# Kernel tuning notes

Hardware: AMD Instinct MI355X
Metric: run time of the kernel (lower is better)

## Reference

```python
import jax, jax.numpy as jnp
import numpy as np

HIDDEN = 2560
HEADS = 32
HEAD_DIM = HIDDEN // HEADS  # 80


def setup_inputs() -> dict:
    key = jax.random.key(0)
    ks = jax.random.split(key, 7)
    B, S, L = 2, 2048, 512
    scale = 1.0 / np.sqrt(HIDDEN)
    return {
        "hidden_states": jax.random.normal(ks[0], (B, S, HIDDEN), jnp.float32),
        "live_state": jax.random.normal(ks[1], (B, L, HIDDEN), jnp.float32),
        # nn.Linear weights stored [out, in]; y = x @ W.T
        "Wq": jax.random.normal(ks[2], (HIDDEN, HIDDEN), jnp.float32) * scale,
        "Wk": jax.random.normal(ks[3], (HIDDEN, HIDDEN), jnp.float32) * scale,
        "Wv": jax.random.normal(ks[4], (HIDDEN, HIDDEN), jnp.float32) * scale,
        "Wo": jax.random.normal(ks[5], (HIDDEN, HIDDEN), jnp.float32) * scale,
        "gate_param": jax.random.normal(ks[6], (), jnp.float32) * 0.1,
    }


def reference(hidden_states, live_state, Wq, Wk, Wv, Wo, gate_param):
    B, S, D = hidden_states.shape
    L = live_state.shape[1]
    H, Dh = HEADS, HEAD_DIM

    q = (hidden_states @ Wq.T).reshape(B, S, H, Dh).transpose(0, 2, 1, 3)  # [B,H,S,Dh]
    k = (live_state @ Wk.T).reshape(B, L, H, Dh).transpose(0, 2, 1, 3)    # [B,H,L,Dh]
    v = (live_state @ Wv.T).reshape(B, L, H, Dh).transpose(0, 2, 1, 3)    # [B,H,L,Dh]

    scale = 1.0 / np.sqrt(Dh)
    scores = jnp.einsum("bhsd,bhld->bhsl", q, k) * scale
    attn_weights = jax.nn.softmax(scores, axis=-1)                        # [B,H,S,L]
    attn_out = jnp.einsum("bhsl,bhld->bhsd", attn_weights, v)
    attn_out = attn_out.transpose(0, 2, 1, 3).reshape(B, S, D)
    attn_out = attn_out @ Wo.T

    gate = jnp.tanh(gate_param)
    output = gate * attn_out
    return output, attn_weights
```

## Files before the change

### kernel.cpp

```cpp
#include <hip/hip_runtime.h>
#include <hip/hip_fp16.h>
#include <cstdint>
#include <cstddef>

#define HID 2560
#define NH  32
#define DHD 80
#define DHP 96
#define NB  2
#define NS  2048
#define NL  512

typedef _Float16 half8_t __attribute__((ext_vector_type(8)));
typedef float f32x4_t __attribute__((ext_vector_type(4)));

__device__ __forceinline__ void gload_lds16(const __half* g, __half* l) {
  __builtin_amdgcn_global_load_lds(
      (const __attribute__((address_space(1))) unsigned int*)g,
      (__attribute__((address_space(3))) unsigned int*)l, 16, 0, 0);
}

__global__ __launch_bounds__(256) void cast_all(const float* __restrict__ X,
                                                const float* __restrict__ LS,
                                                const float* __restrict__ Wq,
                                                const float* __restrict__ Wk,
                                                const float* __restrict__ Wv,
                                                const float* __restrict__ Wo,
                                                __half* __restrict__ Xh,
                                                __half* __restrict__ Lh,
                                                __half* __restrict__ Wqh,
                                                __half* __restrict__ Wkh,
                                                __half* __restrict__ Wvh,
                                                __half* __restrict__ Woh,
                                                __half* __restrict__ Qa,
                                                __half* __restrict__ Ka) {
  const int nX = NB * NS * HID / 4, nL = NB * NL * HID / 4, nW = HID * HID / 4;
  const int ncast = nX + nL + 4 * nW;
  const int qrows = NB * NH * NS, krows = NB * NH * NL;
  const int total = ncast + qrows + krows;
  for (int i = blockIdx.x * 256 + threadIdx.x; i < total; i += gridDim.x * 256) {
    if (i < ncast) {
      const float* src; __half* dst; int off;
      if (i < nX) { src = X; dst = Xh; off = i; }
      else if (i < nX + nL) { src = LS; dst = Lh; off = i - nX; }
      else {
        int j = i - nX - nL;
        int w = j / nW; off = j - w * nW;
        src = (w == 0) ? Wq : (w == 1) ? Wk : (w == 2) ? Wv : Wo;
        dst = (w == 0) ? Wqh : (w == 1) ? Wkh : (w == 2) ? Wvh : Woh;
      }
      float4 v = ((const float4*)src)[off];
      union { __half h[4]; uint2 u; } r;
      r.h[0] = __float2half(v.x);
      r.h[1] = __float2half(v.y);
      r.h[2] = __float2half(v.z);
      r.h[3] = __float2half(v.w);
      ((uint2*)dst)[off] = r.u;
    } else {
      const int j = i - ncast;
      const uint4 z = {0, 0, 0, 0};
      uint4* p = (j < qrows)
          ? (uint4*)(Qa + (size_t)j * DHP + DHD)
          : (uint4*)(Ka + (size_t)(j - qrows) * DHP + DHD);
      p[0] = z; p[1] = z;
    }
  }
}

__device__ __forceinline__ void gemm256_core(const __half* A, const __half* Bt,
                                             int bm, int bn, __half* smem,
                                             f32x4_t (&acc)[8][4]) {
  const int K = HID;
  const int tid  = threadIdx.x;
  const int lane = tid & 63;
  const int wave = tid >> 6;
  const int wr = wave >> 2, wc = wave & 3;
  const int fr = lane & 15, kb = lane >> 4;

  const int sr = tid >> 3;
  const int sj = (tid & 7) ^ (sr & 7);
  const __half* gA = A  + (size_t)(bm * 256 + sr) * K + sj * 8;
  const __half* gB = Bt + (size_t)(bn * 256 + sr) * K + sj * 8;

  auto stage = [&](int h, int kt, int bank) {
    const __half* gbase = (h < 2) ? gA : gB;
    const int rbase = (h & 1) * 128;
#pragma unroll
    for (int i = 0; i < 2; ++i) {
      const __half* g = gbase + (size_t)(rbase + i * 64) * K + (size_t)kt * 64;
      __half* l = smem + bank * 32768 + (h < 2 ? 0 : 16384) + (rbase + i * 64) * 64 + tid * 8;
      gload_lds16(g, l);
    }
  };
  auto rdA = [&](int m, int kk, int bank) -> half8_t {
    const int row = wr * 128 + m * 16 + fr;
    const int off = row * 128 + ((kk * 64 + kb * 16) ^ ((fr & 7) << 4));
    return *(const half8_t*)((const char*)(smem + bank * 32768) + off);
  };
  auto rdB = [&](int n, int kk, int bank) -> half8_t {
    const int row = wc * 64 + n * 16 + fr;
    const int off = row * 128 + ((kk * 64 + kb * 16) ^ ((fr & 7) << 4));
    return *(const half8_t*)((const char*)(smem + bank * 32768 + 16384) + off);
  };

  half8_t af[4][2], bf[4][2];

#pragma unroll
  for (int h = 0; h < 4; ++h) stage(h, 0, 0);

  const int nk = K >> 6;
  for (int kt = 0; kt < nk; ++kt) {
    const int bk = kt & 1, nb2 = bk ^ 1;
    const bool pf = (kt + 1 < nk);

    if (pf) { stage(0, kt + 1, nb2); stage(1, kt + 1, nb2); }
    if (pf) asm volatile("s_waitcnt vmcnt(4)" ::: "memory");
    else    asm volatile("s_waitcnt vmcnt(0)" ::: "memory");
    asm volatile("s_barrier" ::: "memory");
#pragma unroll
    for (int m = 0; m < 4; ++m)
#pragma unroll
      for (int kk = 0; kk < 2; ++kk) af[m][kk] = rdA(m, kk, bk);
#pragma unroll
    for (int n = 0; n < 2; ++n)
#pragma unroll
      for (int kk = 0; kk < 2; ++kk) bf[n][kk] = rdB(n, kk, bk);
    __builtin_amdgcn_s_setprio(1);
#pragma unroll
    for (int m = 0; m < 4; ++m)
#pragma unroll
      for (int n = 0; n < 2; ++n)
#pragma unroll
        for (int kk = 0; kk < 2; ++kk)
          acc[m][n] = __builtin_amdgcn_mfma_f32_16x16x32_f16(af[m][kk], bf[n][kk], acc[m][n], 0, 0, 0);
    __builtin_amdgcn_s_setprio(0);
    asm volatile("s_barrier" ::: "memory");

#pragma unroll
    for (int n = 2; n < 4; ++n)
#pragma unroll
      for (int kk = 0; kk < 2; ++kk) bf[n][kk] = rdB(n, kk, bk);
    if (pf) stage(2, kt + 1, nb2);
    asm volatile("s_barrier" ::: "memory");
    __builtin_amdgcn_s_setprio(1);
#pragma unroll
    for (int m = 0; m < 4; ++m)
#pragma unroll
      for (int n = 2; n < 4; ++n)
#pragma unroll
        for (int kk = 0; kk < 2; ++kk)
          acc[m][n] = __builtin_amdgcn_mfma_f32_16x16x32_f16(af[m][kk], bf[n][kk], acc[m][n], 0, 0, 0);
    __builtin_amdgcn_s_setprio(0);
    asm volatile("s_barrier" ::: "memory");

#pragma unroll
    for (int m = 0; m < 4; ++m)
#pragma unroll
      for (int kk = 0; kk < 2; ++kk) af[m][kk] = rdA(m + 4, kk, bk);
    if (pf) stage(3, kt + 1, nb2);
    asm volatile("s_barrier" ::: "memory");
    __builtin_amdgcn_s_setprio(1);
#pragma unroll
    for (int m = 0; m < 4; ++m)
#pragma unroll
      for (int n = 2; n < 4; ++n)
#pragma unroll
        for (int kk = 0; kk < 2; ++kk)
          acc[m + 4][n] = __builtin_amdgcn_mfma_f32_16x16x32_f16(af[m][kk], bf[n][kk], acc[m + 4][n], 0, 0, 0);
    __builtin_amdgcn_s_setprio(0);
    asm volatile("s_barrier" ::: "memory");

    asm volatile("s_barrier" ::: "memory");
    __builtin_amdgcn_s_setprio(1);
#pragma unroll
    for (int m = 0; m < 4; ++m)
#pragma unroll
      for (int n = 0; n < 2; ++n)
#pragma unroll
        for (int kk = 0; kk < 2; ++kk)
          acc[m + 4][n] = __builtin_amdgcn_mfma_f32_16x16x32_f16(af[m][kk], bf[n][kk], acc[m + 4][n], 0, 0, 0);
    __builtin_amdgcn_s_setprio(0);
    asm volatile("s_barrier" ::: "memory");
  }
}

__global__ __launch_bounds__(512) void fused_qkv(const __half* __restrict__ X,
                                                 const __half* __restrict__ L,
                                                 const __half* __restrict__ Wq,
                                                 const __half* __restrict__ Wk,
                                                 const __half* __restrict__ Wv,
                                                 __half* __restrict__ Qa,
                                                 __half* __restrict__ Ka,
                                                 __half* __restrict__ Va) {
  __shared__ __half smem[2 * 32768];
  int wg = blockIdx.x;
  wg = (wg & 7) * 30 + (wg >> 3);

  int mode, bm, bn;
  const __half *A, *B;
  if (wg < 160)      { mode = 0; A = X; B = Wq; bm = wg / 10;        bn = wg - bm * 10; }
  else if (wg < 200) { mode = 1; A = L; B = Wk; bm = (wg - 160) / 10; bn = (wg - 160) - bm * 10; }
  else               { mode = 2; A = L; B = Wv; bm = (wg - 200) / 10; bn = (wg - 200) - bm * 10; }

  f32x4_t acc[8][4] = {};
  gemm256_core(A, B, bm, bn, smem, acc);

  const int lane = threadIdx.x & 63, wave = threadIdx.x >> 6;
  const int wr = wave >> 2, wc = wave & 3;
  const int fr = lane & 15, kb = lane >> 4;

#pragma unroll
  for (int m = 0; m < 8; ++m)
#pragma unroll
    for (int n = 0; n < 4; ++n)
#pragma unroll
      for (int r = 0; r < 4; ++r) {
        const int row = bm * 256 + wr * 128 + m * 16 + kb * 4 + r;
        const int col = bn * 256 + wc * 64 + n * 16 + fr;
        const float v = acc[m][n][r];
        const int h = col / DHD, d = col - h * DHD;
        if (mode == 0) {
          const int b = row >> 11, s = row & 2047;
          Qa[(((size_t)(b * NH + h)) * NS + s) * DHP + d] =
              __float2half(v * 0.11180339887498949f);
        } else if (mode == 1) {
          const int b = row >> 9, l = row & 511;
          Ka[(((size_t)(b * NH + h)) * NL + l) * DHP + d] = __float2half(v);
        } else {
          const int b = row >> 9, l = row & 511;
          Va[(((size_t)(b * NH + h)) * DHP + d) * NL + l] = __float2half(v);
        }
      }
}

__global__ __launch_bounds__(512) void gemm256_o(const __half* __restrict__ A,
                                                 const __half* __restrict__ Bt,
                                                 float* __restrict__ out,
                                                 const float* __restrict__ gate_p) {
  __shared__ __half smem[2 * 32768];
  int wg = blockIdx.x;
  wg = (wg & 7) * 20 + (wg >> 3);
  const int bm = wg / 10, bn = wg - bm * 10;

  f32x4_t acc[8][4] = {};
  gemm256_core(A, Bt, bm, bn, smem, acc);

  const float gate = tanhf(gate_p[0]);
  const int lane = threadIdx.x & 63, wave = threadIdx.x >> 6;
  const int wr = wave >> 2, wc = wave & 3;
  const int fr = lane & 15, kb = lane >> 4;

#pragma unroll
  for (int m = 0; m < 8; ++m)
#pragma unroll
    for (int n = 0; n < 4; ++n)
#pragma unroll
      for (int r = 0; r < 4; ++r) {
        const int row = bm * 256 + wr * 128 + m * 16 + kb * 4 + r;
        const int col = bn * 256 + wc * 64 + n * 16 + fr;
        __builtin_nontemporal_store(gate * acc[m][n][r],
                                    &out[(size_t)row * HID + col]);
      }
}

__global__ __launch_bounds__(256, 2) void attn_kernel(const __half* __restrict__ Q,
                                                      const __half* __restrict__ Kt,
                                                      const __half* __restrict__ Vt,
                                                      float* __restrict__ P,
                                                      __half* __restrict__ AO) {
  __shared__ __half Pl[4 * 16 * 520];
  __shared__ __half KV[6144];
  const int tid = threadIdx.x;
  const int lane = tid & 63, wave = tid >> 6;
  const int fr = lane & 15, kb = lane >> 4;
  const int bh = blockIdx.y;
  const int r0 = blockIdx.x * 64 + wave * 16;

  const __half* Qb = Q  + ((size_t)bh * NS + r0) * DHP;
  const __half* Kb = Kt + (size_t)bh * NL * DHP;
  const __half* Vb = Vt + (size_t)bh * DHP * NL;

  half8_t aq[3];
#pragma unroll
  for (int kk = 0; kk < 3; ++kk)
    aq[kk] = *(const half8_t*)(Qb + (size_t)fr * DHP + kk * 32 + kb * 8);

  f32x4_t scr[32];

  for (int c = 0; c < 8; ++c) {
#pragma unroll
    for (int i = 0; i < 3; ++i) {
      const int s = (wave * 3 + i) * 64 + lane;
      gload_lds16(Kb + (size_t)c * 64 * DHP + s * 8, KV + s * 8);
    }
    __syncthreads();
#pragma unroll
    for (int ntl = 0; ntl < 4; ++ntl) {
      f32x4_t a = {};
#pragma unroll
      for (int kk = 0; kk < 3; ++kk) {
        half8_t bfv = *(const half8_t*)(KV + (ntl * 16 + fr) * DHP + kk * 32 + kb * 8);
        a = __builtin_amdgcn_mfma_f32_16x16x32_f16(aq[kk], bfv, a, 0, 0, 0);
      }
      scr[c * 4 + ntl] = a;
    }
    __syncthreads();
  }

#pragma unroll
  for (int i = 0; i < 3; ++i) {
    const int s = (wave * 3 + i) * 64 + lane;
    int row = s / 9;
    int col = s - row * 9;
    if (row > 79) row = 79;
    if (col > 7) col = 7;
    gload_lds16(Vb + (size_t)row * NL + col * 8, KV + s * 8);
  }

  __half* Plw = Pl + wave * (16 * 520);
#pragma unroll
  for (int r = 0; r < 4; ++r) {
    float m = -1e30f;
#pragma unroll
    for (int nt = 0; nt < 32; ++nt) m = fmaxf(m, scr[nt][r]);
#pragma unroll
    for (int d = 1; d < 16; d <<= 1) m = fmaxf(m, __shfl_xor(m, d));
    float s = 0.f;
#pragma unroll
    for (int nt = 0; nt < 32; ++nt) {
      float p = __expf(scr[nt][r] - m);
      scr[nt][r] = p;
      s += p;
    }
#pragma unroll
    for (int d = 1; d < 16; d <<= 1) s += __shfl_xor(s, d);
    const float iv = 1.f / s;
#pragma unroll
    for (int nt = 0; nt < 32; ++nt) {
      float p = scr[nt][r] * iv;
      scr[nt][r] = p;
      Plw[(kb * 4 + r) * 520 + nt * 16 + fr] = __float2half(p);
    }
  }

  f32x4_t oc[5] = {};
  for (int c = 0; c < 8; ++c) {
    if (c > 0) {
#pragma unroll
      for (int i = 0; i < 3; ++i) {
        const int s = (wave * 3 + i) * 64 + lane;
        int row = s / 9;
        int col = s - row * 9;
        if (row > 79) row = 79;
        if (col > 7) col = 7;
        gload_lds16(Vb + (size_t)row * NL + c * 64 + col * 8, KV + s * 8);
      }
    }
    __syncthreads();
#pragma unroll
    for (int k0l = 0; k0l < 2; ++k0l) {
      half8_t ap = *(const half8_t*)(Plw + fr * 520 + (c * 2 + k0l) * 32 + kb * 8);
#pragma unroll
      for (int n = 0; n < 5; ++n) {
        half8_t bv = *(const half8_t*)(KV + (n * 16 + fr) * 72 + k0l * 32 + kb * 8);
        oc[n] = __builtin_amdgcn_mfma_f32_16x16x32_f16(ap, bv, oc[n], 0, 0, 0);
      }
    }
    __syncthreads();
  }

  const int b = bh >> 5, h = bh & 31;
#pragma unroll
  for (int n = 0; n < 5; ++n)
#pragma unroll
    for (int r = 0; r < 4; ++r) {
      const int srow = r0 + kb * 4 + r;
      AO[((size_t)b * NS + srow) * HID + h * DHD + n * 16 + fr] = __float2half(oc[n][r]);
    }
#pragma unroll
  for (int r = 0; r < 4; ++r) {
    const int srow = r0 + kb * 4 + r;
    float* Pr = P + ((size_t)bh * NS + srow) * NL;
#pragma unroll
    for (int nt = 0; nt < 32; ++nt)
      __builtin_nontemporal_store(scr[nt][r], &Pr[nt * 16 + fr]);
  }
}

extern "C" void kernel_launch(void* const* d_in, const int* in_sizes, int n_in,
                              void* d_out, int out_size, void* d_ws, size_t ws_size,
                              hipStream_t stream) {
  const float* X  = (const float*)d_in[0];
  const float* LS = (const float*)d_in[1];
  const float* Wq = (const float*)d_in[2];
  const float* Wk = (const float*)d_in[3];
  const float* Wv = (const float*)d_in[4];
  const float* Wo = (const float*)d_in[5];
  const float* gp = (const float*)d_in[6];
  float* out  = (float*)d_out;
  float* Pout = out + (size_t)NB * NS * HID;

  char* w = (char*)d_ws;
  auto alloc = [&](size_t bytes) {
    char* p = w;
    w += (bytes + 255) & ~(size_t)255;
    return p;
  };
  __half* Xh  = (__half*)alloc((size_t)NB * NS * HID * 2);
  __half* Lh  = (__half*)alloc((size_t)NB * NL * HID * 2);
  __half* Wqh = (__half*)alloc((size_t)HID * HID * 2);
  __half* Wkh = (__half*)alloc((size_t)HID * HID * 2);
  __half* Wvh = (__half*)alloc((size_t)HID * HID * 2);
  __half* Woh = (__half*)alloc((size_t)HID * HID * 2);
  __half* Qa  = (__half*)alloc((size_t)NB * NH * NS * DHP * 2);
  __half* Ka  = (__half*)alloc((size_t)NB * NH * NL * DHP * 2);
  __half* Va  = (__half*)alloc((size_t)NB * NH * DHP * NL * 2);
  (void)alloc(4096);
  __half* AOh = Xh;

  cast_all<<<dim3(2048), dim3(256), 0, stream>>>(X, LS, Wq, Wk, Wv, Wo,
                                                 Xh, Lh, Wqh, Wkh, Wvh, Woh,
                                                 Qa, Ka);
  fused_qkv<<<dim3(240), dim3(512), 0, stream>>>(Xh, Lh, Wqh, Wkh, Wvh, Qa, Ka, Va);
  attn_kernel<<<dim3(NS / 64, NB * NH), dim3(256), 0, stream>>>(
      Qa, Ka, Va, Pout, AOh);
  gemm256_o<<<dim3(160), dim3(512), 0, stream>>>(AOh, Woh, out, gp);
}
```

Baseline: 305.2 us.

## Retile output projection GEMM to 256x160 tiles over 256 workgroups

Replaces the 256x256-tile output projection GEMM (160 workgroups) with a dedicated 256x160-tile kernel launched on 256 workgroups. The aim is better coverage of the GPU's compute units and less tail imbalance. The new kernel has its own double-buffered LDS pipeline: XOR-swizzled direct global-to-LDS loads, prefetch of the next K tile interleaved between MFMA phases, and setprio around the MFMA bursts. The smaller N tile lowers arithmetic intensity per workgroup, and the many barriers add synchronisation overhead.

```diff
diff --git a/kernel.cpp b/kernel.cpp
--- a/kernel.cpp
+++ b/kernel.cpp
@@ -233,31 +233,146 @@
       }
 }
 
-__global__ __launch_bounds__(512) void gemm256_o(const __half* __restrict__ A,
+__global__ __launch_bounds__(512) void gemm160_o(const __half* __restrict__ A,
                                                  const __half* __restrict__ Bt,
                                                  float* __restrict__ out,
                                                  const float* __restrict__ gate_p) {
-  __shared__ __half smem[2 * 32768];
+  __shared__ __half smem[2 * 26624];
+  const int K = HID;
   int wg = blockIdx.x;
-  wg = (wg & 7) * 20 + (wg >> 3);
-  const int bm = wg / 10, bn = wg - bm * 10;
-
-  f32x4_t acc[8][4] = {};
-  gemm256_core(A, Bt, bm, bn, smem, acc);
+  wg = (wg & 7) * 32 + (wg >> 3);
+  const int bm = wg >> 4, bn = wg & 15;
+
+  const int tid  = threadIdx.x;
+  const int lane = tid & 63;
+  const int wave = tid >> 6;
+  const int wr = wave >> 1, wc = wave & 1;
+  const int fr = lane & 15, kb = lane >> 4;
+
+  const int sr = tid >> 3;
+  const int sj = (tid & 7) ^ (sr & 7);
+  const __half* gA = A + (size_t)(bm * 256 + sr) * K + sj * 8;
+
+  auto stageA = [&](int h, int kt, int bank) {
+    const int rbase = h * 128;
+#pragma unroll
+    for (int i = 0; i < 2; ++i) {
+      const __half* g = gA + (size_t)(rbase + i * 64) * K + (size_t)kt * 64;
+      __half* l = smem + bank * 26624 + (rbase + i * 64) * 64 + tid * 8;
+      gload_lds16(g, l);
+    }
+  };
+  auto stageB = [&](int c, int kt, int bank) {
+    if (c < 2 || tid < 256) {
+      const int s = c * 512 + tid;
+      const int row = s >> 3;
+      const int j = (tid & 7) ^ (row & 7);
+      const __half* g = Bt + (size_t)(bn * 160 + row) * K + (size_t)kt * 64 + j * 8;
+      __half* l = smem + bank * 26624 + 16384 + s * 8;
+      gload_lds16(g, l);
+    }
+  };
+  auto rdA = [&](int m, int kk, int bank) -> half8_t {
+    const int row = wr * 64 + m * 16 + fr;
+    const int off = row * 128 + ((kk * 64 + kb * 16) ^ ((fr & 7) << 4));
+    return *(const half8_t*)((const char*)(smem + bank * 26624) + off);
+  };
+  auto rdB = [&](int n, int kk, int bank) -> half8_t {
+    const int row = wc * 80 + n * 16 + fr;
+    const int off = row * 128 + ((kk * 64 + kb * 16) ^ ((fr & 7) << 4));
+    return *(const half8_t*)((const char*)(smem + bank * 26624 + 16384) + off);
+  };
+
+  f32x4_t acc[4][5] = {};
+  half8_t af[2][2], bf[5][2];
+
+  stageA(0, 0, 0); stageA(1, 0, 0);
+  stageB(0, 0, 0); stageB(1, 0, 0); stageB(2, 0, 0);
+
+  const int nk = K >> 6;
+  for (int kt = 0; kt < nk; ++kt) {
+    const int bk = kt & 1, nb2 = bk ^ 1;
+    const bool pf = (kt + 1 < nk);
+
+    if (pf) { stageA(0, kt + 1, nb2); stageA(1, kt + 1, nb2); }
+    if (pf) asm volatile("s_waitcnt vmcnt(4)" ::: "memory");
+    else    asm volatile("s_waitcnt vmcnt(0)" ::: "memory");
+    asm volatile("s_barrier" ::: "memory");
+#pragma unroll
+    for (int m = 0; m < 2; ++m)
+#pragma unroll
+      for (int kk = 0; kk < 2; ++kk) af[m][kk] = rdA(m, kk, bk);
+#pragma unroll
+    for (int n = 0; n < 3; ++n)
+#pragma unroll
+      for (int kk = 0; kk < 2; ++kk) bf[n][kk] = rdB(n, kk, bk);
+    __builtin_amdgcn_s_setprio(1);
+#pragma unroll
+    for (int m = 0; m < 2; ++m)
+#pragma unroll
+      for (int n = 0; n < 3; ++n)
+#pragma unroll
+        for (int kk = 0; kk < 2; ++kk)
+          acc[m][n] = __builtin_amdgcn_mfma_f32_16x16x32_f16(af[m][kk], bf[n][kk], acc[m][n], 0, 0, 0);
+    __builtin_amdgcn_s_setprio(0);
+    asm volatile("s_barrier" ::: "memory");
+
+#pragma unroll
+    for (int n = 3; n < 5; ++n)
+#pragma unroll
+      for (int kk = 0; kk < 2; ++kk) bf[n][kk] = rdB(n, kk, bk);
+    if (pf) { stageB(0, kt + 1, nb2); stageB(1, kt + 1, nb2); }
+    asm volatile("s_barrier" ::: "memory");
+    __builtin_amdgcn_s_setprio(1);
+#pragma unroll
+    for (int m = 0; m < 2; ++m)
+#pragma unroll
+      for (int n = 3; n < 5; ++n)
+#pragma unroll
+        for (int kk = 0; kk < 2; ++kk)
+          acc[m][n] = __builtin_amdgcn_mfma_f32_16x16x32_f16(af[m][kk], bf[n][kk], acc[m][n], 0, 0, 0);
+    __builtin_amdgcn_s_setprio(0);
+    asm volatile("s_barrier" ::: "memory");
+
+#pragma unroll
+    for (int m = 0; m < 2; ++m)
+#pragma unroll
+      for (int kk = 0; kk < 2; ++kk) af[m][kk] = rdA(m + 2, kk, bk);
+    if (pf) stageB(2, kt + 1, nb2);
+    asm volatile("s_barrier" ::: "memory");
+    __builtin_amdgcn_s_setprio(1);
+#pragma unroll
+    for (int m = 0; m < 2; ++m)
+#pragma unroll
+      for (int n = 3; n < 5; ++n)
+#pragma unroll
+        for (int kk = 0; kk < 2; ++kk)
+          acc[m + 2][n] = __builtin_amdgcn_mfma_f32_16x16x32_f16(af[m][kk], bf[n][kk], acc[m + 2][n], 0, 0, 0);
+    __builtin_amdgcn_s_setprio(0);
+    asm volatile("s_barrier" ::: "memory");
+
+    asm volatile("s_barrier" ::: "memory");
+    __builtin_amdgcn_s_setprio(1);
+#pragma unroll
+    for (int m = 0; m < 2; ++m)
+#pragma unroll
+      for (int n = 0; n < 3; ++n)
+#pragma unroll
+        for (int kk = 0; kk < 2; ++kk)
+          acc[m + 2][n] = __builtin_amdgcn_mfma_f32_16x16x32_f16(af[m][kk], bf[n][kk], acc[m + 2][n], 0, 0, 0);
+    __builtin_amdgcn_s_setprio(0);
+    asm volatile("s_barrier" ::: "memory");
+  }
 
   const float gate = tanhf(gate_p[0]);
-  const int lane = threadIdx.x & 63, wave = threadIdx.x >> 6;
-  const int wr = wave >> 2, wc = wave & 3;
-  const int fr = lane & 15, kb = lane >> 4;
-
-#pragma unroll
-  for (int m = 0; m < 8; ++m)
-#pragma unroll
-    for (int n = 0; n < 4; ++n)
+#pragma unroll
+  for (int m = 0; m < 4; ++m)
+#pragma unroll
+    for (int n = 0; n < 5; ++n)
 #pragma unroll
       for (int r = 0; r < 4; ++r) {
-        const int row = bm * 256 + wr * 128 + m * 16 + kb * 4 + r;
-        const int col = bn * 256 + wc * 64 + n * 16 + fr;
+        const int row = bm * 256 + wr * 64 + m * 16 + kb * 4 + r;
+        const int col = bn * 160 + wc * 80 + n * 16 + fr;
         __builtin_nontemporal_store(gate * acc[m][n][r],
                                     &out[(size_t)row * HID + col]);
       }
@@ -424,5 +539,5 @@
   fused_qkv<<<dim3(240), dim3(512), 0, stream>>>(Xh, Lh, Wqh, Wkh, Wvh, Qa, Ka, Va);
   attn_kernel<<<dim3(NS / 64, NB * NH), dim3(256), 0, stream>>>(
       Qa, Ka, Va, Pout, AOh);
-  gemm256_o<<<dim3(160), dim3(512), 0, stream>>>(AOh, Woh, out, gp);
-}
+  gemm160_o<<<dim3(256), dim3(512), 0, stream>>>(AOh, Woh, out, gp);
+}
```

New measurement: 292.2 us. 4.3% less time.
